# Performance work log

Measured on AMD Instinct MI355X. Metric: run time of the kernel, lower is better.

The kernel has to match this reference:

```python
import jax, jax.numpy as jnp
import numpy as np

EPS = 1e-5
K = 16
DILATION = 1

def _bn(x, g, b, axes):
    # BatchNorm in training mode: batch statistics over all axes except channel (last)
    m = jnp.mean(x, axis=axes, keepdims=True)
    v = jnp.var(x, axis=axes, keepdims=True)
    return (x - m) * jax.lax.rsqrt(v + EPS) * g + b

def _knn_idx(p, q, k):
    # p: [B,N,3], q: [B,M,3] -> indices [B,M,k] of nearest points in p for each q
    d = (jnp.sum(q * q, -1)[:, :, None]
         - 2.0 * jnp.einsum('bmc,bnc->bmn', q, p)
         + jnp.sum(p * p, -1)[:, None, :])  # [B,M,N]
    _, idx = jax.lax.top_k(-d, k)
    return jax.lax.stop_gradient(idx)

def setup_inputs() -> dict:
    key = jax.random.key(0)
    ks = jax.random.split(key, 16)
    B, N, M, Cin, Cout = 8, 8192, 2048, 64, 128
    mid, K2 = Cout // 4, K * K
    s = 0.02
    d = {
        'p': jax.random.normal(ks[0], (B, N, 3), jnp.float32),
        'q': jax.random.normal(ks[1], (B, M, 3), jnp.float32),
        'x': jax.random.normal(ks[2], (B, Cin, N), jnp.float32),
        # mlp: two 1x1 convs (3->mid->mid) each with BN
        'W1': jax.random.normal(ks[3], (mid, 3), jnp.float32) * s,
        'b1': jnp.zeros((mid,), jnp.float32),
        'g1': jnp.ones((mid,), jnp.float32), 'be1': jnp.zeros((mid,), jnp.float32),
        'W2': jax.random.normal(ks[4], (mid, mid), jnp.float32) * s,
        'b2': jnp.zeros((mid,), jnp.float32),
        'g2': jnp.ones((mid,), jnp.float32), 'be2': jnp.zeros((mid,), jnp.float32),
        # stn: conv [1,K] (3->K^2), then two 1x1 convs (K^2->K^2)
        'Ws1': jax.random.normal(ks[5], (K2, 3, K), jnp.float32) * s,
        'bs1': jnp.zeros((K2,), jnp.float32),
        'gs1': jnp.ones((K2,), jnp.float32), 'bes1': jnp.zeros((K2,), jnp.float32),
        'Ws2': jax.random.normal(ks[6], (K2, K2), jnp.float32) * s,
        'bs2': jnp.zeros((K2,), jnp.float32),
        'gs2': jnp.ones((K2,), jnp.float32), 'bes2': jnp.zeros((K2,), jnp.float32),
        'Ws3': jax.random.normal(ks[7], (K2, K2), jnp.float32) * s,
        'bs3': jnp.zeros((K2,), jnp.float32),
        # final conv [1,K]: (Cin+mid -> Cout) with BN
        'Wc': jax.random.normal(ks[8], (Cout, Cin + mid, K), jnp.float32) * s,
        'bc': jnp.zeros((Cout,), jnp.float32),
        'gc': jnp.ones((Cout,), jnp.float32), 'bec': jnp.zeros((Cout,), jnp.float32),
    }
    return d

def reference(p, q, x, W1, b1, g1, be1, W2, b2, g2, be2,
              Ws1, bs1, gs1, bes1, Ws2, bs2, gs2, bes2, Ws3, bs3,
              Wc, bc, gc, bec):
    B, M = q.shape[0], q.shape[1]
    idx = _knn_idx(p, q, K * DILATION)[..., ::DILATION]  # [B,M,K]
    # gather neighbor coords and center: p_hat [B,M,K,3]
    p_n = jax.vmap(lambda a, i: a[i])(p, idx)
    p_hat = p_n - q[:, :, None, :]
    # mlp (pointwise convs, channel-last)
    h = jax.nn.relu(_bn(jnp.einsum('bmkc,oc->bmko', p_hat, W1) + b1, g1, be1, (0, 1, 2)))
    h = jax.nn.relu(_bn(jnp.einsum('bmkc,oc->bmko', h, W2) + b2, g2, be2, (0, 1, 2)))
    # gather features: x [B,Cin,N] -> [B,M,K,Cin]
    xt = jnp.transpose(x, (0, 2, 1))
    x_n = jax.vmap(lambda a, i: a[i])(xt, idx)
    x_hat = jnp.concatenate([h, x_n], axis=-1)  # [B,M,K,mid+Cin]
    # stn -> transform T [B,M,K,K]
    t = jax.nn.relu(_bn(jnp.einsum('bmkc,ock->bmo', p_hat, Ws1) + bs1, gs1, bes1, (0, 1)))
    t = jax.nn.relu(_bn(jnp.einsum('bmi,oi->bmo', t, Ws2) + bs2, gs2, bes2, (0, 1)))
    t = jnp.einsum('bmi,oi->bmo', t, Ws3) + bs3  # [B,M,K*K]
    T = t.reshape(B, M, K, K)
    x2 = jnp.einsum('bmij,bmjc->bmic', T, x_hat)  # [B,M,K,mid+Cin]
    out = jax.nn.relu(_bn(jnp.einsum('bmkc,ock->bmo', x2, Wc) + bc, gc, bec, (0, 1)))  # [B,M,Cout]
    return (q, jnp.transpose(out, (0, 2, 1)))  # q, x:[B,Cout,M]
```

## Files before the change

kernel.cpp:

```cpp
#include <hip/hip_runtime.h>
#include <hip/hip_bf16.h>


#define EPS 1e-5f

constexpr int Bb   = 8;
constexpr int Np   = 8192;
constexpr int Mq   = 2048;
constexpr int COUT = 128;
constexpr int BM   = Bb * Mq;
constexpr int BMK  = BM * 16;
constexpr int GC   = 16;
constexpr int NC   = GC * GC * GC;
constexpr int CAP  = 320;

typedef __attribute__((ext_vector_type(8))) short short8;
typedef __attribute__((ext_vector_type(4))) float f32x4;

__device__ __forceinline__ unsigned short f2bf(float x) {
  unsigned u = __float_as_uint(x);
  u += 0x7fffu + ((u >> 16) & 1u);
  return (unsigned short)(u >> 16);
}
__device__ __forceinline__ float bf2f_lo(unsigned v) { return __uint_as_float(v << 16); }
__device__ __forceinline__ float bf2f_hi(unsigned v) { return __uint_as_float(v & 0xffff0000u); }

__device__ __forceinline__ int cell_of(float c) {
  int v = (int)floorf(c * 2.0f + 8.0f);
  return v < 0 ? 0 : (v > 15 ? 15 : v);
}

__device__ __forceinline__ unsigned enc_dist(float d) {
  unsigned uu = __float_as_uint(d);
  return uu ^ (((unsigned)(((int)uu) >> 31)) | 0x80000000u);
}

__device__ __forceinline__ void bsort64(unsigned long long& v, int lane) {
#pragma unroll
  for (int k = 2; k <= 64; k <<= 1) {
#pragma unroll
    for (int jj = k >> 1; jj > 0; jj >>= 1) {
      unsigned long long o = __shfl_xor(v, jj);
      bool keepMin = (((lane & k) == 0) == ((lane & jj) == 0));
      unsigned long long mn = v < o ? v : o;
      unsigned long long mx = v < o ? o : v;
      v = keepMin ? mn : mx;
    }
  }
}
__device__ __forceinline__ void bmerge64(unsigned long long& v, int lane) {
#pragma unroll
  for (int jj = 32; jj > 0; jj >>= 1) {
    unsigned long long o = __shfl_xor(v, jj);
    bool keepMin = ((lane & jj) == 0);
    unsigned long long mn = v < o ? v : o;
    unsigned long long mx = v < o ? o : v;
    v = keepMin ? mn : mx;
  }
}
__device__ __forceinline__ unsigned long long sort_smallest64(const unsigned long long* buf,
                                                              int C, int lane) {
  unsigned long long run = (lane < C) ? buf[lane] : ~0ULL;
  bsort64(run, lane);
  for (int b2 = 64; b2 < C; b2 += 64) {
    unsigned long long v = (b2 + lane < C) ? buf[b2 + lane] : ~0ULL;
    bsort64(v, lane);
    unsigned long long vr = __shfl_xor(v, 63);
    unsigned long long m = run < vr ? run : vr;
    bmerge64(m, lane);
    run = m;
  }
  return run;
}


__device__ __forceinline__ void bn1_compute(int o, const float* __restrict__ st,
                                            const float* __restrict__ W1,
                                            const float* __restrict__ b1,
                                            const float* __restrict__ g1,
                                            const float* __restrict__ be1,
                                            float* sc_out, float* shf_out) {
  float n = (float)BMK;
  float w0 = W1[3 * o], w1 = W1[3 * o + 1], w2 = W1[3 * o + 2], b = b1[o];
  float s0 = st[0], s1 = st[1], s2 = st[2];
  float m00 = st[3], m11 = st[4], m22 = st[5], m01 = st[6], m02 = st[7], m12 = st[8];
  float ws = (w0 * s0 + w1 * s1 + w2 * s2) / n;
  float mean = b + ws;
  float quad = w0 * w0 * m00 + w1 * w1 * m11 + w2 * w2 * m22 +
               2.f * (w0 * w1 * m01 + w0 * w2 * m02 + w1 * w2 * m12);
  float ex2 = quad / n + 2.f * b * ws + b * b;
  float var = ex2 - mean * mean;
  float sc = g1[o] * rsqrtf(var + EPS);
  *sc_out = sc;
  *shf_out = be1[o] - mean * sc + b * sc;
}

__global__ __launch_bounds__(256) void prep_kernel(const float* __restrict__ p,
                                                   const float* __restrict__ x,
                                                   const float* __restrict__ Wc,
                                                   const float* __restrict__ Ws1,
                                                   float4* __restrict__ pp4,
                                                   float* __restrict__ xt,
                                                   unsigned short* __restrict__ wcrp,
                                                   unsigned short* __restrict__ ws1r,
                                                   int* __restrict__ hist) {
  __shared__ float tile[64][65];
  int blk = blockIdx.x;
  int tid = threadIdx.x;
  if (blk < 256) {
    int i = blk * 256 + tid;
    float px = p[3 * i], py = p[3 * i + 1], pz = p[3 * i + 2];
    float pp = __fadd_rn(__fadd_rn(__fmul_rn(px, px), __fmul_rn(py, py)), __fmul_rn(pz, pz));
    pp4[i] = make_float4(px, py, pz, pp);
    int b = i >> 13;
    int cid = (cell_of(px) << 8) | (cell_of(py) << 4) | cell_of(pz);
    atomicAdd(&hist[b * NC + cid], 1);
  } else if (blk < 1280) {
    int bx = blk - 256;
    int b = bx >> 7;
    int n0 = (bx & 127) << 6;
    int nl = tid & 63;
    int r0 = tid >> 6;
    const float* xb = x + (size_t)b * 64 * Np;
    for (int c = r0; c < 64; c += 4) tile[c][nl] = xb[(size_t)c * Np + n0 + nl];
    __syncthreads();
    float* xtb = xt + (size_t)b * Np * 64;
    for (int n = r0; n < 64; n += 4) xtb[(size_t)(n0 + n) * 64 + nl] = tile[nl][n];
  } else if (blk < 2048) {
    int g = (blk - 1280) * 256 + tid;
    if (g < 128 * 1536) {
      int o = g / 1536, r = g % 1536;
      int c = r % 96, j = r / 96;
      wcrp[g] = f2bf(Wc[(size_t)o * 1536 + c * 16 + j]);
    }
  } else {
    int g = (blk - 2048) * 256 + tid;
    int o = g >> 6, i = g & 63;
    float val = 0.f;
    if (i < 48) {
      int k = i / 3, c = i - 3 * k;
      val = Ws1[(size_t)o * 48 + c * 16 + k];
    }
    unsigned short h = f2bf(val);
    float hf = __uint_as_float(((unsigned)h) << 16);
    unsigned short l = f2bf(val - hf);
    ws1r[g] = h;
    ws1r[16384 + g] = l;
  }
}

__global__ __launch_bounds__(256) void prefix_kernel(const int* __restrict__ hist,
                                                     int* __restrict__ cellstart,
                                                     int* __restrict__ cursor) {
  __shared__ int ls[256];
  int b = blockIdx.x, t = threadIdx.x;
  const int* h = hist + b * NC;
  int loc[16], s = 0;
#pragma unroll
  for (int k = 0; k < 16; ++k) { loc[k] = h[t * 16 + k]; s += loc[k]; }
  ls[t] = s;
  __syncthreads();
  for (int off = 1; off < 256; off <<= 1) {
    int v = (t >= off) ? ls[t - off] : 0;
    __syncthreads();
    ls[t] += v;
    __syncthreads();
  }
  int run = ls[t] - s;
  int* cs = cellstart + b * (NC + 1);
  int* cu = cursor + b * NC;
#pragma unroll
  for (int k = 0; k < 16; ++k) {
    cs[t * 16 + k] = run;
    cu[t * 16 + k] = run;
    run += loc[k];
  }
  if (t == 255) cs[NC] = run;
}

__global__ __launch_bounds__(256) void scatter_kernel(const float4* __restrict__ pp4,
                                                      int* __restrict__ cursor,
                                                      float4* __restrict__ sp4,
                                                      int* __restrict__ sidx) {
  int i = blockIdx.x * 256 + threadIdx.x;
  int b = i >> 13;
  float4 pv = pp4[i];
  int cid = (cell_of(pv.x) << 8) | (cell_of(pv.y) << 4) | cell_of(pv.z);
  int pos = atomicAdd(&cursor[b * NC + cid], 1);
  sp4[(size_t)b * Np + pos] = pv;
  sidx[(size_t)b * Np + pos] = i & 8191;
}

__global__ __launch_bounds__(256) void knn_kernel(const float4* __restrict__ pp4,
                                                  const float4* __restrict__ sp4,
                                                  const int* __restrict__ sidx,
                                                  const int* __restrict__ cellstart,
                                                  const float* __restrict__ q,
                                                  int* __restrict__ idx_out) {
  __shared__ unsigned long long cand[8][CAP];
  int tid = threadIdx.x;
  int wslot = tid >> 6;
  int wave = blockIdx.x * 4 + wslot;
  int lane = tid & 63;
  int q0 = wave * 2;
  int b = q0 >> 11;
  const float4* pb = pp4 + (size_t)b * Np;
  const float4* sp = sp4 + (size_t)b * Np;
  const int* sx = sidx + (size_t)b * Np;
  const int* cs = cellstart + b * (NC + 1);
  float qx[2], qy[2], qz[2], qqv[2];
#pragma unroll
  for (int j = 0; j < 2; ++j) {
    const float* qp = q + (size_t)(q0 + j) * 3;
    qx[j] = qp[0]; qy[j] = qp[1]; qz[j] = qp[2];
    qqv[j] = __fadd_rn(__fadd_rn(__fmul_rn(qx[j], qx[j]), __fmul_rn(qy[j], qy[j])),
                       __fmul_rn(qz[j], qz[j]));
  }
  float tau_f[2] = {INFINITY, INFINITY};

  for (int j = 0; j < 2; ++j) {
    int cx = cell_of(qx[j]), cy = cell_of(qy[j]), cz = cell_of(qz[j]);
    int alo = 0, blo = 0, nbw = 1, ncols = 1, zlo = 0, zhi = 0;
    int myS = 0, myE = 0;
    for (int r = 0;; ++r) {
      alo = cx - r; if (alo < 0) alo = 0;
      int ahi = cx + r; if (ahi > 15) ahi = 15;
      blo = cy - r; if (blo < 0) blo = 0;
      int bhi = cy + r; if (bhi > 15) bhi = 15;
      zlo = cz - r; if (zlo < 0) zlo = 0;
      zhi = cz + r; if (zhi > 15) zhi = 15;
      nbw = bhi - blo + 1;
      ncols = (ahi - alo + 1) * nbw;
      int total = 0;
      for (int l0 = 0; l0 < ncols; l0 += 64) {
        int l = l0 + lane;
        int sL = 0, eL = 0;
        if (l < ncols) {
          int da = l / nbw, db = l - da * nbw;
          int cbase = ((alo + da) << 8) | ((blo + db) << 4);
          sL = cs[cbase + zlo];
          eL = cs[cbase + zhi + 1];
        }
        if (l0 == 0) { myS = sL; myE = eL; }
        total += eL - sL;
      }
#pragma unroll
      for (int o = 32; o > 0; o >>= 1) total += __shfl_xor(total, o);
      if (total >= 16 || r >= 15) break;
    }
    unsigned u0 = 0xFFFFFFFFu, u1 = 0xFFFFFFFFu;
    int wcnt = 0;
    int ccen = (cx - alo) * nbw + (cy - blo);
    for (int c2 = 0; c2 < ncols && wcnt < 128; ++c2) {
      int cc = (c2 == 0) ? ccen : (c2 <= ccen ? c2 - 1 : c2);
      int s0, e;
      if (cc < 64) {
        s0 = __shfl(myS, cc);
        e = __shfl(myE, cc);
      } else {
        int da = cc / nbw, db = cc - da * nbw;
        int cbase = ((alo + da) << 8) | ((blo + db) << 4);
        s0 = cs[cbase + zlo];
        e = cs[cbase + zhi + 1];
      }
      for (int off = s0; off < e && wcnt < 128; off += 64) {
        int rem = e - off; if (rem > 64) rem = 64;
        int rot = wcnt & 63;
        int rel = (lane - rot) & 63;
        int g = wcnt + rel;
        if (rel < rem && g < 128) {
          float4 pv = sp[off + rel];
          float ee = __fmaf_rn(qz[j], pv.z, __fmaf_rn(qy[j], pv.y, __fmul_rn(qx[j], pv.x)));
          float d = __fadd_rn(__fsub_rn(qqv[j], __fmul_rn(2.0f, ee)), pv.w);
          unsigned uu = enc_dist(d);
          if (g < 64) u0 = uu; else u1 = uu;
        }
        wcnt += rem;
      }
    }
    unsigned lo = 0u, hi = 0xFF800000u;
    for (int it = 0; it < 20; ++it) {
      unsigned mid = lo + ((hi - lo) >> 1);
      int c = (int)__popcll(__ballot(u0 <= mid)) + (int)__popcll(__ballot(u1 <= mid));
      if (c >= 16) hi = mid; else lo = mid + 1;
    }
    tau_f[j] = (hi >= 0x80000000u) ? __uint_as_float(hi ^ 0x80000000u)
                                   : __uint_as_float(~hi);
  }

  int cnt[2] = {0, 0};
  unsigned long long lanebelow = (1ULL << lane) - 1ULL;
  for (int j = 0; j < 2; ++j) {
    float R = sqrtf(fmaxf(tau_f[j], 0.f) + 3e-5f) * 1.0005f;
    int ax0 = cell_of(qx[j] - R), ax1 = cell_of(qx[j] + R);
    int ay0 = cell_of(qy[j] - R), ay1 = cell_of(qy[j] + R);
    int az0 = cell_of(qz[j] - R), az1 = cell_of(qz[j] + R);
    int nby = ay1 - ay0 + 1;
    int ncols = (ax1 - ax0 + 1) * nby;
    int myS = 0, myE = 0;
    if (lane < ncols) {
      int da = lane / nby, db = lane - da * nby;
      int cbase = ((ax0 + da) << 8) | ((ay0 + db) << 4);
      myS = cs[cbase + az0];
      myE = cs[cbase + az1 + 1];
    }
    for (int cc = 0; cc < ncols; ++cc) {
      int s0, e;
      if (cc < 64) {
        s0 = __shfl(myS, cc);
        e = __shfl(myE, cc);
      } else {
        int da = cc / nby, db = cc - da * nby;
        int cbase = ((ax0 + da) << 8) | ((ay0 + db) << 4);
        s0 = cs[cbase + az0];
        e = cs[cbase + az1 + 1];
      }
      for (int off = s0; off < e; off += 64) {
        int pos = off + lane;
        bool valid = pos < e;
        float4 pv = sp[valid ? pos : s0];
        float ee = __fmaf_rn(qz[j], pv.z, __fmaf_rn(qy[j], pv.y, __fmul_rn(qx[j], pv.x)));
        float d = __fadd_rn(__fsub_rn(qqv[j], __fmul_rn(2.0f, ee)), pv.w);
        if (!valid) d = __uint_as_float(0x7FC00000u);
        unsigned long long mask = __ballot(d <= tau_f[j]);
        if (mask) {
          if (d <= tau_f[j]) {
            int oi = sx[pos];
            unsigned uu = enc_dist(d);
            int wp = cnt[j] + (int)__popcll(mask & lanebelow);
            if (wp < CAP)
              cand[wslot * 2 + j][wp] = (((unsigned long long)uu) << 32) | (unsigned)oi;
          }
          cnt[j] += (int)__popcll(mask);
        }
      }
    }
  }
  __syncthreads();

  for (int j = 0; j < 2; ++j) {
    int slot = wslot * 2 + j;
    if (cnt[j] <= CAP) {
      unsigned long long run = sort_smallest64(&cand[slot][0], cnt[j], lane);
      if (lane < 16)
        idx_out[(size_t)(q0 + j) * 16 + lane] = (int)(run & 0xffffffffULL);
    } else {
      unsigned long long kk = ~0ULL;
      float tl = tau_f[j];
      for (int base = 0; base < Np; base += 64) {
        float4 pv = pb[base + lane];
        float ee = __fmaf_rn(qz[j], pv.z, __fmaf_rn(qy[j], pv.y, __fmul_rn(qx[j], pv.x)));
        float dv = __fadd_rn(__fsub_rn(qqv[j], __fmul_rn(2.0f, ee)), pv.w);
        unsigned long long mask = __ballot(dv <= tl);
        if (mask) {
          unsigned uu = enc_dist(dv);
          unsigned long long cd = (((unsigned long long)uu) << 32) | (unsigned)(base + lane);
          do {
            int src = __ffsll((unsigned long long)mask) - 1;
            mask &= mask - 1;
            unsigned long long ck = __shfl(cd, src);
            unsigned long long up = __shfl_up(kk, 1);
            if (lane == 0) up = 0ULL;
            if (lane < 16 && ck < kk) kk = (up > ck) ? up : ck;
          } while (mask);
          unsigned long long tt = __shfl(kk, 15);
          unsigned tm = (unsigned)(tt >> 32);
          unsigned inv2 = tm ^ ((tm & 0x80000000u) ? 0x80000000u : 0xFFFFFFFFu);
          float tc = (tm == 0xFFFFFFFFu) ? INFINITY : __uint_as_float(inv2);
          if (tc < tl) tl = tc;
        }
      }
      if (lane < 16)
        idx_out[(size_t)(q0 + j) * 16 + lane] = (int)(kk & 0xffffffffULL);
    }
  }
}

__global__ __launch_bounds__(256) void phat_stats_kernel(const float4* __restrict__ pp4,
                                                         const float* __restrict__ q,
                                                         const int* __restrict__ idx,
                                                         float* __restrict__ phat,
                                                         float* __restrict__ stats) {
  float a[9];
#pragma unroll
  for (int k = 0; k < 9; ++k) a[k] = 0.f;
  int tid = threadIdx.x;
  for (int it = 0; it < 4; ++it) {
    int bmk = blockIdx.x * 256 + tid + it * 65536;
    int bm = bmk >> 4;
    int b = bm >> 11;
    int j = idx[bmk];
    float4 pv = pp4[(size_t)b * Np + j];
    const float* qp = q + (size_t)bm * 3;
    float h0 = pv.x - qp[0], h1 = pv.y - qp[1], h2 = pv.z - qp[2];
    phat[(size_t)bmk * 3 + 0] = h0;
    phat[(size_t)bmk * 3 + 1] = h1;
    phat[(size_t)bmk * 3 + 2] = h2;
    a[0] += h0; a[1] += h1; a[2] += h2;
    a[3] += h0 * h0; a[4] += h1 * h1; a[5] += h2 * h2;
    a[6] += h0 * h1; a[7] += h0 * h2; a[8] += h1 * h2;
  }
#pragma unroll
  for (int off = 32; off > 0; off >>= 1)
#pragma unroll
    for (int k = 0; k < 9; ++k) a[k] += __shfl_down(a[k], off);
  __shared__ float ls[9];
  if (tid < 9) ls[tid] = 0.f;
  __syncthreads();
  if ((tid & 63) == 0)
    for (int k = 0; k < 9; ++k) atomicAdd(&ls[k], a[k]);
  __syncthreads();
  if (tid < 9) atomicAdd(&stats[tid], ls[tid]);
}

__global__ __launch_bounds__(256) void stats2_kernel(const float* __restrict__ phat,
                                                     const float* __restrict__ stats,
                                                     const float* __restrict__ W1,
                                                     const float* __restrict__ b1,
                                                     const float* __restrict__ g1,
                                                     const float* __restrict__ be1,
                                                     const float* __restrict__ W2,
                                                     const float* __restrict__ b2,
                                                     float* __restrict__ stats2) {
  __shared__ float hsh[256 * 36];
  __shared__ float w2s[32 * 33];
  __shared__ float w1s[96], sc1[32], sh1[32], b2s[32], ls[64];
  int tid = threadIdx.x;
  if (tid < 32) {
    bn1_compute(tid, stats, W1, b1, g1, be1, &sc1[tid], &sh1[tid]);
    b2s[tid] = b2[tid];
  }
  if (tid < 96) w1s[tid] = W1[tid];
  if (tid < 64) ls[tid] = 0.f;
  for (int e = tid; e < 1024; e += 256) w2s[(e >> 5) * 33 + (e & 31)] = W2[e];
  __syncthreads();
  {
    int bmk = blockIdx.x * 256 + tid;
    float h0 = phat[(size_t)bmk * 3], hy = phat[(size_t)bmk * 3 + 1], hz = phat[(size_t)bmk * 3 + 2];
#pragma unroll
    for (int o4 = 0; o4 < 8; ++o4) {
      float4 r;
      float* rp = (float*)&r;
#pragma unroll
      for (int u = 0; u < 4; ++u) {
        int o = o4 * 4 + u;
        float t = w1s[3 * o] * h0 + w1s[3 * o + 1] * hy + w1s[3 * o + 2] * hz;
        rp[u] = fmaxf(0.f, t * sc1[o] + sh1[o]);
      }
      *(float4*)&hsh[tid * 36 + o4 * 4] = r;
    }
  }
  __syncthreads();
  int oc = tid & 31, grp = tid >> 5;
  float wrow[32];
#pragma unroll
  for (int c = 0; c < 32; ++c) wrow[c] = w2s[oc * 33 + c];
  float bias = b2s[oc];
  float ss = 0.f, qq = 0.f;
  for (int r = 0; r < 32; ++r) {
    int row = grp * 32 + r;
    float a = bias;
    const float4* hr = (const float4*)&hsh[row * 36];
#pragma unroll
    for (int c4 = 0; c4 < 8; ++c4) {
      float4 hv = hr[c4];
      a += hv.x * wrow[c4 * 4 + 0];
      a += hv.y * wrow[c4 * 4 + 1];
      a += hv.z * wrow[c4 * 4 + 2];
      a += hv.w * wrow[c4 * 4 + 3];
    }
    ss += a;
    qq += a * a;
  }
  atomicAdd(&ls[oc], ss);
  atomicAdd(&ls[32 + oc], qq);
  __syncthreads();
  if (tid < 64) atomicAdd(&stats2[tid], ls[tid]);
}

__global__ __launch_bounds__(256) void stn1_kernel(const float* __restrict__ phat,
                                                   const unsigned short* __restrict__ ws1r,
                                                   const float* __restrict__ bs1,
                                                   float* __restrict__ pt1,
                                                   float* __restrict__ spt1) {
  __shared__ unsigned short Ah[64 * 72], Al[64 * 72], Bh[128 * 72], Bl[128 * 72];
  __shared__ float ls[256];
  int tid = threadIdx.x;
  ls[tid] = 0.f;
  int mb = blockIdx.x >> 1, nb = blockIdx.x & 1;
  int bm0 = mb * 64, o0 = nb * 128;
  {
    int zr = tid >> 2, zc = 48 + (tid & 3) * 4;
    *(unsigned long long*)&Ah[zr * 72 + zc] = 0ULL;
    *(unsigned long long*)&Al[zr * 72 + zc] = 0ULL;
  }
  {
    int ar = tid >> 2, aseg = tid & 3;
    const float* Ap = phat + (size_t)(bm0 + ar) * 48 + aseg * 12;
    float4 v0 = *(const float4*)(Ap);
    float4 v1 = *(const float4*)(Ap + 4);
    float4 v2 = *(const float4*)(Ap + 8);
    float av[12] = {v0.x, v0.y, v0.z, v0.w, v1.x, v1.y, v1.z, v1.w, v2.x, v2.y, v2.z, v2.w};
    unsigned long long ph[3] = {0ULL, 0ULL, 0ULL}, pl[3] = {0ULL, 0ULL, 0ULL};
#pragma unroll
    for (int t = 0; t < 12; ++t) {
      unsigned short h = f2bf(av[t]);
      float hf = __uint_as_float(((unsigned)h) << 16);
      unsigned short l = f2bf(av[t] - hf);
      ph[t >> 2] |= ((unsigned long long)h) << ((t & 3) * 16);
      pl[t >> 2] |= ((unsigned long long)l) << ((t & 3) * 16);
    }
    int base = ar * 72 + aseg * 12;
#pragma unroll
    for (int t4 = 0; t4 < 3; ++t4) {
      *(unsigned long long*)&Ah[base + t4 * 4] = ph[t4];
      *(unsigned long long*)&Al[base + t4 * 4] = pl[t4];
    }
  }
#pragma unroll
  for (int pass = 0; pass < 4; ++pass) {
    int g = pass * 2048 + tid * 8;
    int br = g >> 6, i2 = g & 63;
    short8 vh = *(const short8*)&ws1r[(size_t)(o0 + br) * 64 + i2];
    short8 vl = *(const short8*)&ws1r[16384 + (size_t)(o0 + br) * 64 + i2];
    *(short8*)&Bh[br * 72 + i2] = vh;
    *(short8*)&Bl[br * 72 + i2] = vl;
  }
  __syncthreads();
  int wid = tid >> 6, lane = tid & 63;
  int wm = wid >> 1, wn = wid & 1;
  int mh = lane & 15, quad = lane >> 4;
  f32x4 acc[2][4];
#pragma unroll
  for (int a = 0; a < 2; ++a)
#pragma unroll
    for (int bq = 0; bq < 4; ++bq) acc[a][bq] = (f32x4){0.f, 0.f, 0.f, 0.f};
#pragma unroll
  for (int kc = 0; kc < 2; ++kc) {
    int ko = kc * 32 + quad * 8;
#pragma unroll
    for (int mt = 0; mt < 2; ++mt) {
      short8 ah = *(const short8*)&Ah[(wm * 32 + mt * 16 + mh) * 72 + ko];
      short8 al = *(const short8*)&Al[(wm * 32 + mt * 16 + mh) * 72 + ko];
#pragma unroll
      for (int nt = 0; nt < 4; ++nt) {
        short8 bh = *(const short8*)&Bh[(wn * 64 + nt * 16 + mh) * 72 + ko];
        short8 bl = *(const short8*)&Bl[(wn * 64 + nt * 16 + mh) * 72 + ko];
        acc[mt][nt] = __builtin_amdgcn_mfma_f32_16x16x32_bf16(ah, bh, acc[mt][nt], 0, 0, 0);
        acc[mt][nt] = __builtin_amdgcn_mfma_f32_16x16x32_bf16(ah, bl, acc[mt][nt], 0, 0, 0);
        acc[mt][nt] = __builtin_amdgcn_mfma_f32_16x16x32_bf16(al, bh, acc[mt][nt], 0, 0, 0);
      }
    }
  }
#pragma unroll
  for (int mt = 0; mt < 2; ++mt)
#pragma unroll
    for (int nt = 0; nt < 4; ++nt) {
      int colL = wn * 64 + nt * 16 + mh;
      int col = o0 + colL;
      float bvv = bs1[col];
      float ps = 0.f, pq = 0.f;
#pragma unroll
      for (int r = 0; r < 4; ++r) {
        float val = acc[mt][nt][r] + bvv;
        pt1[(size_t)(bm0 + wm * 32 + mt * 16 + quad * 4 + r) * 256 + col] = val;
        ps += val;
        pq += val * val;
      }
      atomicAdd(&ls[colL], ps);
      atomicAdd(&ls[128 + colL], pq);
    }
  __syncthreads();
  if (tid < 128) {
    atomicAdd(&spt1[o0 + tid], ls[tid]);
    atomicAdd(&spt1[256 + o0 + tid], ls[128 + tid]);
  }
}

__global__ __launch_bounds__(256) void stn_mm_kernel(const float* __restrict__ in,
                                                     const float* __restrict__ sums,
                                                     const float* __restrict__ gg,
                                                     const float* __restrict__ be,
                                                     const float* __restrict__ W,
                                                     const float* __restrict__ bias,
                                                     float* __restrict__ out,
                                                     float* __restrict__ outstats,
                                                     int do_stats) {
  __shared__ unsigned short As[64 * 40], Bs[128 * 40];
  __shared__ float scA[256], shA[256], ls[256];
  int tid = threadIdx.x;
  ls[tid] = 0.f;
  {
    float n = (float)BM;
    float mean = sums[tid] / n;
    float var = sums[256 + tid] / n - mean * mean;
    float s = gg[tid] * rsqrtf(var + EPS);
    scA[tid] = s;
    shA[tid] = be[tid] - mean * s;
  }
  int mb = blockIdx.x >> 1, nb = blockIdx.x & 1;
  int bm0 = mb * 64, o0 = nb * 128;
  int wid = tid >> 6, lane = tid & 63;
  int wm = wid >> 1, wn = wid & 1;
  int mh = lane & 15, quad = lane >> 4;
  f32x4 acc[2][4];
#pragma unroll
  for (int a = 0; a < 2; ++a)
#pragma unroll
    for (int bq = 0; bq < 4; ++bq) acc[a][bq] = (f32x4){0.f, 0.f, 0.f, 0.f};
  int ar = tid >> 2, aseg = tid & 3;
  const float* Ag = in + (size_t)(bm0 + ar) * 256 + aseg * 8;
  int aoff = ar * 40 + aseg * 8;
  int ci = aseg * 8;
  for (int i0 = 0; i0 < 256; i0 += 32) {
    __syncthreads();
    float4 v0 = *(const float4*)(Ag + i0);
    float4 v1 = *(const float4*)(Ag + i0 + 4);
    float av[8] = {v0.x, v0.y, v0.z, v0.w, v1.x, v1.y, v1.z, v1.w};
    short8 ap;
#pragma unroll
    for (int k = 0; k < 8; ++k)
      ap[k] = (short)f2bf(fmaxf(0.f, av[k] * scA[i0 + ci + k] + shA[i0 + ci + k]));
    *(short8*)&As[aoff] = ap;
#pragma unroll
    for (int jb = 0; jb < 2; ++jb) {
      int br = jb * 64 + ar;
      const float* Bg = W + (size_t)(o0 + br) * 256 + aseg * 8;
      float4 u0 = *(const float4*)(Bg + i0);
      float4 u1 = *(const float4*)(Bg + i0 + 4);
      float bv[8] = {u0.x, u0.y, u0.z, u0.w, u1.x, u1.y, u1.z, u1.w};
      short8 bp;
#pragma unroll
      for (int k = 0; k < 8; ++k) bp[k] = (short)f2bf(bv[k]);
      *(short8*)&Bs[br * 40 + aseg * 8] = bp;
    }
    __syncthreads();
#pragma unroll
    for (int mt = 0; mt < 2; ++mt) {
      short8 af = *(const short8*)&As[(wm * 32 + mt * 16 + mh) * 40 + quad * 8];
#pragma unroll
      for (int nt = 0; nt < 4; ++nt) {
        short8 bf = *(const short8*)&Bs[(wn * 64 + nt * 16 + mh) * 40 + quad * 8];
        acc[mt][nt] = __builtin_amdgcn_mfma_f32_16x16x32_bf16(af, bf, acc[mt][nt], 0, 0, 0);
      }
    }
  }
#pragma unroll
  for (int mt = 0; mt < 2; ++mt)
#pragma unroll
    for (int nt = 0; nt < 4; ++nt) {
      int colL = wn * 64 + nt * 16 + mh;
      int col = o0 + colL;
      float bvv = bias[col];
      float ps = 0.f, pq = 0.f;
#pragma unroll
      for (int r = 0; r < 4; ++r) {
        float val = acc[mt][nt][r] + bvv;
        out[(size_t)(bm0 + wm * 32 + mt * 16 + quad * 4 + r) * 256 + col] = val;
        ps += val;
        pq += val * val;
      }
      if (do_stats) {
        atomicAdd(&ls[colL], ps);
        atomicAdd(&ls[128 + colL], pq);
      }
    }
  if (do_stats) {
    __syncthreads();
    if (tid < 128) {
      atomicAdd(&outstats[o0 + tid], ls[tid]);
      atomicAdd(&outstats[256 + o0 + tid], ls[128 + tid]);
    }
  }
}

__global__ __launch_bounds__(256) void xhat_x2_kernel(const float* __restrict__ phat,
                                                      const float* __restrict__ stats,
                                                      const float* __restrict__ stats2,
                                                      const float* __restrict__ W1,
                                                      const float* __restrict__ b1,
                                                      const float* __restrict__ g1,
                                                      const float* __restrict__ be1,
                                                      const float* __restrict__ W2,
                                                      const float* __restrict__ b2,
                                                      const float* __restrict__ g2,
                                                      const float* __restrict__ be2,
                                                      const float* __restrict__ xt,
                                                      const int* __restrict__ idx,
                                                      const float* __restrict__ Tbuf,
                                                      unsigned short* __restrict__ x2) {
  __shared__ unsigned xh[256 * 17];
  __shared__ float w1s[96], w2s[32 * 33], sc1[32], sh1[32], sc2[32], sh2[32];
  int tid = threadIdx.x;
  if (tid < 32) {
    bn1_compute(tid, stats, W1, b1, g1, be1, &sc1[tid], &sh1[tid]);
    float n = (float)BMK;
    float mean = stats2[tid] / n;
    float var = stats2[32 + tid] / n - mean * mean;
    float s = g2[tid] * rsqrtf(var + EPS);
    sc2[tid] = s;
    sh2[tid] = be2[tid] - mean * s + b2[tid] * s;
  }
  if (tid < 96) w1s[tid] = W1[tid];
  for (int e = tid; e < 1024; e += 256) w2s[(e >> 5) * 33 + (e & 31)] = W2[e];
  __syncthreads();
  int bm0 = blockIdx.x * 16;
  int b = bm0 >> 11;
  int bml = tid >> 4, j = tid & 15;
  int bmk = (bm0 + bml) * 16 + j;
  unsigned h2p[16];
  {
    float h0 = phat[(size_t)bmk * 3], hy = phat[(size_t)bmk * 3 + 1], hz = phat[(size_t)bmk * 3 + 2];
    float h1v[32];
#pragma unroll
    for (int o = 0; o < 32; ++o) {
      float t = w1s[3 * o] * h0 + w1s[3 * o + 1] * hy + w1s[3 * o + 2] * hz;
      h1v[o] = fmaxf(0.f, t * sc1[o] + sh1[o]);
    }
#pragma unroll
    for (int o4 = 0; o4 < 8; ++o4) {
      float r[4];
#pragma unroll
      for (int u = 0; u < 4; ++u) {
        int o = o4 * 4 + u;
        float a = 0.f;
#pragma unroll
        for (int c = 0; c < 32; ++c) a += h1v[c] * w2s[o * 33 + c];
        r[u] = fmaxf(0.f, a * sc2[o] + sh2[o]);
      }
      h2p[o4 * 2] = (unsigned)f2bf(r[0]) | (((unsigned)f2bf(r[1])) << 16);
      h2p[o4 * 2 + 1] = (unsigned)f2bf(r[2]) | (((unsigned)f2bf(r[3])) << 16);
    }
  }
  int jx = idx[bmk];
  const float4* xr = (const float4*)(xt + ((size_t)b * Np + jx) * 64);
  float Tr[16];
  {
    const float4* tg = (const float4*)(Tbuf + (size_t)(bm0 + bml) * 256 + j * 16);
#pragma unroll
    for (int w4 = 0; w4 < 4; ++w4) {
      float4 tv = tg[w4];
      Tr[w4 * 4 + 0] = tv.x; Tr[w4 * 4 + 1] = tv.y;
      Tr[w4 * 4 + 2] = tv.z; Tr[w4 * 4 + 3] = tv.w;
    }
  }
  unsigned* dst32 = (unsigned*)(x2 + (size_t)bmk * 96);
#pragma unroll
  for (int ch = 0; ch < 3; ++ch) {
    if (ch == 0) {
#pragma unroll
      for (int t = 0; t < 16; ++t) xh[tid * 17 + t] = h2p[t];
    } else {
      float4 xv[8];
#pragma unroll
      for (int t = 0; t < 8; ++t) xv[t] = xr[(ch - 1) * 8 + t];
#pragma unroll
      for (int t = 0; t < 8; ++t) {
        xh[tid * 17 + t * 2] = (unsigned)f2bf(xv[t].x) | (((unsigned)f2bf(xv[t].y)) << 16);
        xh[tid * 17 + t * 2 + 1] = (unsigned)f2bf(xv[t].z) | (((unsigned)f2bf(xv[t].w)) << 16);
      }
    }
    __syncthreads();
    float acc[32];
#pragma unroll
    for (int cc = 0; cc < 32; ++cc) acc[cc] = 0.f;
#pragma unroll
    for (int jj = 0; jj < 16; ++jj) {
      const unsigned* xr2 = &xh[(bml * 16 + jj) * 17];
      float t = Tr[jj];
#pragma unroll
      for (int cc = 0; cc < 16; ++cc) {
        unsigned uv = xr2[cc];
        acc[cc * 2] += t * bf2f_lo(uv);
        acc[cc * 2 + 1] += t * bf2f_hi(uv);
      }
    }
#pragma unroll
    for (int cc = 0; cc < 16; ++cc)
      dst32[ch * 16 + cc] = (unsigned)f2bf(acc[cc * 2]) | (((unsigned)f2bf(acc[cc * 2 + 1])) << 16);
    __syncthreads();
  }
}

__global__ __launch_bounds__(256) void preout_kernel(const unsigned short* __restrict__ x2,
                                                     const unsigned short* __restrict__ Wcrp,
                                                     const float* __restrict__ bc,
                                                     float* __restrict__ pout,
                                                     float* __restrict__ spout) {
  __shared__ unsigned short As[64 * 40], Bs[128 * 40];
  __shared__ float ls[256];
  int tid = threadIdx.x;
  ls[tid] = 0.f;
  int bm0 = blockIdx.x * 64;
  int wid = tid >> 6, lane = tid & 63;
  int wm = wid >> 1, wn = wid & 1;
  int mh = lane & 15, quad = lane >> 4;
  f32x4 acc[2][4];
#pragma unroll
  for (int a = 0; a < 2; ++a)
#pragma unroll
    for (int bq = 0; bq < 4; ++bq) acc[a][bq] = (f32x4){0.f, 0.f, 0.f, 0.f};
  int ar = tid >> 2, aseg = tid & 3;
  const unsigned short* Ag = x2 + (size_t)(bm0 + ar) * 1536 + aseg * 8;
  const unsigned short* Bg0 = Wcrp + (size_t)ar * 1536 + aseg * 8;
  const unsigned short* Bg1 = Wcrp + (size_t)(64 + ar) * 1536 + aseg * 8;
  int aoff = ar * 40 + aseg * 8;
  short8 a_pre = *(const short8*)Ag;
  short8 b_pre0 = *(const short8*)Bg0;
  short8 b_pre1 = *(const short8*)Bg1;
  for (int i0 = 0; i0 < 1536; i0 += 32) {
    __syncthreads();
    *(short8*)&As[aoff] = a_pre;
    *(short8*)&Bs[aoff] = b_pre0;
    *(short8*)&Bs[64 * 40 + aoff] = b_pre1;
    __syncthreads();
    if (i0 + 32 < 1536) {
      a_pre = *(const short8*)(Ag + i0 + 32);
      b_pre0 = *(const short8*)(Bg0 + i0 + 32);
      b_pre1 = *(const short8*)(Bg1 + i0 + 32);
    }
#pragma unroll
    for (int mt = 0; mt < 2; ++mt) {
      short8 af = *(const short8*)&As[(wm * 32 + mt * 16 + mh) * 40 + quad * 8];
#pragma unroll
      for (int nt = 0; nt < 4; ++nt) {
        short8 bf = *(const short8*)&Bs[(wn * 64 + nt * 16 + mh) * 40 + quad * 8];
        acc[mt][nt] = __builtin_amdgcn_mfma_f32_16x16x32_bf16(af, bf, acc[mt][nt], 0, 0, 0);
      }
    }
  }
#pragma unroll
  for (int mt = 0; mt < 2; ++mt)
#pragma unroll
    for (int nt = 0; nt < 4; ++nt) {
      int col = wn * 64 + nt * 16 + mh;
      float bvv = bc[col];
      float ps = 0.f, pq = 0.f;
#pragma unroll
      for (int r = 0; r < 4; ++r) {
        float val = acc[mt][nt][r] + bvv;
        pout[(size_t)(bm0 + wm * 32 + mt * 16 + quad * 4 + r) * 128 + col] = val;
        ps += val;
        pq += val * val;
      }
      atomicAdd(&ls[col], ps);
      atomicAdd(&ls[128 + col], pq);
    }
  __syncthreads();
  atomicAdd(&spout[tid], ls[tid]);
}

__global__ __launch_bounds__(256) void final_kernel(const float* __restrict__ q,
                                                    const float* __restrict__ pout,
                                                    const float* __restrict__ scs,
                                                    const float* __restrict__ gc,
                                                    const float* __restrict__ bec,
                                                    float* __restrict__ dout) {
  __shared__ float ldsT[128 * 65];
  int blk = blockIdx.x;
  int tid = threadIdx.x;
  if (blk < 192) {
    int g = blk * 256 + tid;
    dout[g] = q[g];
    return;
  }
  int blk2 = blk - 192;
  int b = blk2 >> 5;
  int m0 = (blk2 & 31) * 64;
  int row = tid >> 2, seg = tid & 3;
  const float4* src = (const float4*)(pout + ((size_t)(b * Mq) + m0 + row) * 128 + seg * 32);
#pragma unroll
  for (int k4 = 0; k4 < 8; ++k4) {
    float4 v = src[k4];
    int o = seg * 32 + k4 * 4;
    ldsT[(o + 0) * 65 + row] = v.x;
    ldsT[(o + 1) * 65 + row] = v.y;
    ldsT[(o + 2) * 65 + row] = v.z;
    ldsT[(o + 3) * 65 + row] = v.w;
  }
  __syncthreads();
  int lane = tid & 63, wv = tid >> 6;
  float n = (float)BM;
  float* base = dout + (size_t)BM * 3 + (size_t)b * COUT * Mq + m0;
#pragma unroll
  for (int rep = 0; rep < 32; ++rep) {
    int o = wv * 32 + rep;
    float mean = scs[o] / n;
    float var = scs[128 + o] / n - mean * mean;
    float s = gc[o] * rsqrtf(var + EPS);
    float shv = bec[o] - mean * s;
    float v = ldsT[o * 65 + lane];
    base[(size_t)o * Mq + lane] = fmaxf(0.f, v * s + shv);
  }
}

extern "C" void kernel_launch(void* const* d_in, const int* in_sizes, int n_in, void* d_out,
                              int out_size, void* d_ws, size_t ws_size, hipStream_t stream) {
  const float* p = (const float*)d_in[0];
  const float* q = (const float*)d_in[1];
  const float* x = (const float*)d_in[2];
  const float* W1 = (const float*)d_in[3];
  const float* b1 = (const float*)d_in[4];
  const float* g1 = (const float*)d_in[5];
  const float* be1 = (const float*)d_in[6];
  const float* W2 = (const float*)d_in[7];
  const float* b2 = (const float*)d_in[8];
  const float* g2 = (const float*)d_in[9];
  const float* be2 = (const float*)d_in[10];
  const float* Ws1 = (const float*)d_in[11];
  const float* bs1 = (const float*)d_in[12];
  const float* gs1 = (const float*)d_in[13];
  const float* bes1 = (const float*)d_in[14];
  const float* Ws2 = (const float*)d_in[15];
  const float* bs2 = (const float*)d_in[16];
  const float* gs2 = (const float*)d_in[17];
  const float* bes2 = (const float*)d_in[18];
  const float* Ws3 = (const float*)d_in[19];
  const float* bs3 = (const float*)d_in[20];
  const float* Wc = (const float*)d_in[21];
  const float* bc = (const float*)d_in[22];
  const float* gc = (const float*)d_in[23];
  const float* bec = (const float*)d_in[24];
  float* dout = (float*)d_out;

  char* ws = (char*)d_ws;
  float* stats = (float*)ws;
  size_t off = 8192;
  float4* pp4 = (float4*)(ws + off);  off += (size_t)Bb * Np * 16;
  int* idxb = (int*)(ws + off);       off += (size_t)BMK * 4;
  float* xt = (float*)(ws + off);     off += (size_t)Bb * Np * 64 * 4;
  float* phat = (float*)(ws + off);   off += (size_t)BMK * 3 * 4;
  float* pt1 = (float*)(ws + off);    off += (size_t)BM * 256 * 4;
  float* pt2 = (float*)(ws + off);    off += (size_t)BM * 256 * 4;
  float* Tb = (float*)(ws + off);     off += (size_t)BM * 256 * 4;
  float* pout = (float*)(ws + off);   off += (size_t)BM * 128 * 4;
  unsigned short* wcrp = (unsigned short*)(ws + off); off += (size_t)1536 * 128 * 2;
  unsigned short* x2 = (unsigned short*)(ws + off);   off += (size_t)BM * 1536 * 2;
  int* hist = (int*)(ws + off);       off += (size_t)Bb * NC * 4;
  int* cursor = (int*)(ws + off);     off += (size_t)Bb * NC * 4;
  int* cellstart = (int*)(ws + off);  off += (size_t)Bb * (NC + 1) * 4;
  float4* sp4 = (float4*)(ws + off);  off += (size_t)Bb * Np * 16;
  int* sidx = (int*)(ws + off);       off += (size_t)Bb * Np * 4;
  unsigned short* ws1r = (unsigned short*)(ws + off); off += (size_t)2 * 256 * 64 * 2;

  hipMemsetAsync(stats, 0, 8192, stream);
  hipMemsetAsync(hist, 0, (size_t)Bb * NC * 4, stream);
  hipLaunchKernelGGL(prep_kernel, dim3(2112), dim3(256), 0, stream, p, x, Wc, Ws1, pp4, xt, wcrp, ws1r, hist);
  hipLaunchKernelGGL(prefix_kernel, dim3(8), dim3(256), 0, stream, hist, cellstart, cursor);
  hipLaunchKernelGGL(scatter_kernel, dim3(256), dim3(256), 0, stream, pp4, cursor, sp4, sidx);
  hipLaunchKernelGGL(knn_kernel, dim3(2048), dim3(256), 0, stream, pp4, sp4, sidx, cellstart, q, idxb);
  hipLaunchKernelGGL(phat_stats_kernel, dim3(256), dim3(256), 0, stream, pp4, q, idxb, phat, stats);
  hipLaunchKernelGGL(stn1_kernel, dim3(512), dim3(256), 0, stream, phat, ws1r, bs1, pt1, stats + 128);
  hipLaunchKernelGGL(stats2_kernel, dim3(1024), dim3(256), 0, stream, phat, stats, W1, b1, g1, be1, W2, b2, stats + 16);
  hipLaunchKernelGGL(stn_mm_kernel, dim3(512), dim3(256), 0, stream, pt1, stats + 128, gs1, bes1, Ws2, bs2, pt2, stats + 640, 1);
  hipLaunchKernelGGL(stn_mm_kernel, dim3(512), dim3(256), 0, stream, pt2, stats + 640, gs2, bes2, Ws3, bs3, Tb, (float*)nullptr, 0);
  hipLaunchKernelGGL(xhat_x2_kernel, dim3(1024), dim3(256), 0, stream, phat, stats, stats + 16,
                     W1, b1, g1, be1, W2, b2, g2, be2, xt, idxb, Tb, x2);
  hipLaunchKernelGGL(preout_kernel, dim3(256), dim3(256), 0, stream, x2, wcrp, bc, pout, stats + 1152);
  hipLaunchKernelGGL(final_kernel, dim3(448), dim3(256), 0, stream, q, pout, stats + 1152, gc, bec, dout);
}
```

Baseline: 379.9 us.

## Restructure T·x_hat product so each thread owns a channel column, not a row

Each thread now computes one channel pair (or quad) for all 16 output neighbours of its query, instead of one output row across all channels. T rows are staged in shared memory, and neighbour features are gathered straight from global memory as contiguous float4s with bf16 rounding. Only one sync is needed now, the three-chunk xh staging loop is gone, and the W1/W2 shared-memory copies are replaced by direct global reads. The cost is less coalesced global loads and stores (each thread writes strided 4-byte words across 16 rows) and more shared reads of T.

```diff
diff --git a/kernel.cpp b/kernel.cpp
--- a/kernel.cpp
+++ b/kernel.cpp
@@ -24,6 +24,9 @@
 }
 __device__ __forceinline__ float bf2f_lo(unsigned v) { return __uint_as_float(v << 16); }
 __device__ __forceinline__ float bf2f_hi(unsigned v) { return __uint_as_float(v & 0xffff0000u); }
+__device__ __forceinline__ float bfround(float x) {
+  return __uint_as_float(((unsigned)f2bf(x)) << 16);
+}
 
 __device__ __forceinline__ int cell_of(float c) {
   int v = (int)floorf(c * 2.0f + 8.0f);
@@ -690,7 +693,8 @@
                                                       const float* __restrict__ Tbuf,
                                                       unsigned short* __restrict__ x2) {
   __shared__ unsigned xh[256 * 17];
-  __shared__ float w1s[96], w2s[32 * 33], sc1[32], sh1[32], sc2[32], sh2[32];
+  __shared__ float Tst[256 * 16];
+  __shared__ float sc1[32], sh1[32], sc2[32], sh2[32];
   int tid = threadIdx.x;
   if (tid < 32) {
     bn1_compute(tid, stats, W1, b1, g1, be1, &sc1[tid], &sh1[tid]);
@@ -701,20 +705,17 @@
     sc2[tid] = s;
     sh2[tid] = be2[tid] - mean * s + b2[tid] * s;
   }
-  if (tid < 96) w1s[tid] = W1[tid];
-  for (int e = tid; e < 1024; e += 256) w2s[(e >> 5) * 33 + (e & 31)] = W2[e];
   __syncthreads();
   int bm0 = blockIdx.x * 16;
   int b = bm0 >> 11;
   int bml = tid >> 4, j = tid & 15;
   int bmk = (bm0 + bml) * 16 + j;
-  unsigned h2p[16];
   {
     float h0 = phat[(size_t)bmk * 3], hy = phat[(size_t)bmk * 3 + 1], hz = phat[(size_t)bmk * 3 + 2];
     float h1v[32];
 #pragma unroll
     for (int o = 0; o < 32; ++o) {
-      float t = w1s[3 * o] * h0 + w1s[3 * o + 1] * hy + w1s[3 * o + 2] * hz;
+      float t = W1[3 * o] * h0 + W1[3 * o + 1] * hy + W1[3 * o + 2] * hz;
       h1v[o] = fmaxf(0.f, t * sc1[o] + sh1[o]);
     }
 #pragma unroll
@@ -725,60 +726,71 @@
         int o = o4 * 4 + u;
         float a = 0.f;
 #pragma unroll
-        for (int c = 0; c < 32; ++c) a += h1v[c] * w2s[o * 33 + c];
+        for (int c = 0; c < 32; ++c) a += h1v[c] * W2[o * 32 + c];
         r[u] = fmaxf(0.f, a * sc2[o] + sh2[o]);
       }
-      h2p[o4 * 2] = (unsigned)f2bf(r[0]) | (((unsigned)f2bf(r[1])) << 16);
-      h2p[o4 * 2 + 1] = (unsigned)f2bf(r[2]) | (((unsigned)f2bf(r[3])) << 16);
-    }
-  }
-  int jx = idx[bmk];
-  const float4* xr = (const float4*)(xt + ((size_t)b * Np + jx) * 64);
-  float Tr[16];
+      xh[tid * 17 + o4 * 2] = (unsigned)f2bf(r[0]) | (((unsigned)f2bf(r[1])) << 16);
+      xh[tid * 17 + o4 * 2 + 1] = (unsigned)f2bf(r[2]) | (((unsigned)f2bf(r[3])) << 16);
+    }
+    const float4* tg = (const float4*)(Tbuf + (size_t)(bm0 + bml) * 256 + j * 16);
+    float4* td = (float4*)&Tst[tid * 16];
+    td[0] = tg[0]; td[1] = tg[1]; td[2] = tg[2]; td[3] = tg[3];
+  }
+  __syncthreads();
+  int cl = j;
   {
-    const float4* tg = (const float4*)(Tbuf + (size_t)(bm0 + bml) * 256 + j * 16);
-#pragma unroll
-    for (int w4 = 0; w4 < 4; ++w4) {
-      float4 tv = tg[w4];
-      Tr[w4 * 4 + 0] = tv.x; Tr[w4 * 4 + 1] = tv.y;
-      Tr[w4 * 4 + 2] = tv.z; Tr[w4 * 4 + 3] = tv.w;
-    }
-  }
-  unsigned* dst32 = (unsigned*)(x2 + (size_t)bmk * 96);
-#pragma unroll
-  for (int ch = 0; ch < 3; ++ch) {
-    if (ch == 0) {
-#pragma unroll
-      for (int t = 0; t < 16; ++t) xh[tid * 17 + t] = h2p[t];
-    } else {
-      float4 xv[8];
-#pragma unroll
-      for (int t = 0; t < 8; ++t) xv[t] = xr[(ch - 1) * 8 + t];
-#pragma unroll
-      for (int t = 0; t < 8; ++t) {
-        xh[tid * 17 + t * 2] = (unsigned)f2bf(xv[t].x) | (((unsigned)f2bf(xv[t].y)) << 16);
-        xh[tid * 17 + t * 2 + 1] = (unsigned)f2bf(xv[t].z) | (((unsigned)f2bf(xv[t].w)) << 16);
-      }
-    }
-    __syncthreads();
-    float acc[32];
-#pragma unroll
-    for (int cc = 0; cc < 32; ++cc) acc[cc] = 0.f;
+    float vlo[16], vhi[16];
 #pragma unroll
     for (int jj = 0; jj < 16; ++jj) {
-      const unsigned* xr2 = &xh[(bml * 16 + jj) * 17];
-      float t = Tr[jj];
-#pragma unroll
-      for (int cc = 0; cc < 16; ++cc) {
-        unsigned uv = xr2[cc];
-        acc[cc * 2] += t * bf2f_lo(uv);
-        acc[cc * 2 + 1] += t * bf2f_hi(uv);
-      }
-    }
-#pragma unroll
-    for (int cc = 0; cc < 16; ++cc)
-      dst32[ch * 16 + cc] = (unsigned)f2bf(acc[cc * 2]) | (((unsigned)f2bf(acc[cc * 2 + 1])) << 16);
-    __syncthreads();
+      unsigned uv = xh[(bml * 16 + jj) * 17 + cl];
+      vlo[jj] = bf2f_lo(uv);
+      vhi[jj] = bf2f_hi(uv);
+    }
+    for (int jo = 0; jo < 16; ++jo) {
+      const float4* tr4 = (const float4*)&Tst[(bml * 16 + jo) * 16];
+      float4 ta = tr4[0], tb = tr4[1], tc = tr4[2], tdd = tr4[3];
+      float trow[16] = {ta.x, ta.y, ta.z, ta.w, tb.x, tb.y, tb.z, tb.w,
+                        tc.x, tc.y, tc.z, tc.w, tdd.x, tdd.y, tdd.z, tdd.w};
+      float a0 = 0.f, a1 = 0.f;
+#pragma unroll
+      for (int jj = 0; jj < 16; ++jj) {
+        a0 += trow[jj] * vlo[jj];
+        a1 += trow[jj] * vhi[jj];
+      }
+      unsigned* dst = (unsigned*)(x2 + (size_t)((bm0 + bml) * 16 + jo) * 96);
+      dst[cl] = (unsigned)f2bf(a0) | (((unsigned)f2bf(a1)) << 16);
+    }
+  }
+  {
+    const int* idxrow = idx + (size_t)(bm0 + bml) * 16;
+    float v0[16], v1[16], v2[16], v3[16];
+#pragma unroll
+    for (int jj = 0; jj < 16; ++jj) {
+      int jx = idxrow[jj];
+      float4 xv = *(const float4*)(xt + ((size_t)b * Np + jx) * 64 + cl * 4);
+      v0[jj] = bfround(xv.x);
+      v1[jj] = bfround(xv.y);
+      v2[jj] = bfround(xv.z);
+      v3[jj] = bfround(xv.w);
+    }
+    for (int jo = 0; jo < 16; ++jo) {
+      const float4* tr4 = (const float4*)&Tst[(bml * 16 + jo) * 16];
+      float4 ta = tr4[0], tb = tr4[1], tc = tr4[2], tdd = tr4[3];
+      float trow[16] = {ta.x, ta.y, ta.z, ta.w, tb.x, tb.y, tb.z, tb.w,
+                        tc.x, tc.y, tc.z, tc.w, tdd.x, tdd.y, tdd.z, tdd.w};
+      float a0 = 0.f, a1 = 0.f, a2 = 0.f, a3 = 0.f;
+#pragma unroll
+      for (int jj = 0; jj < 16; ++jj) {
+        float t = trow[jj];
+        a0 += t * v0[jj];
+        a1 += t * v1[jj];
+        a2 += t * v2[jj];
+        a3 += t * v3[jj];
+      }
+      unsigned* dst = (unsigned*)(x2 + (size_t)((bm0 + bml) * 16 + jo) * 96);
+      dst[16 + cl * 2] = (unsigned)f2bf(a0) | (((unsigned)f2bf(a1)) << 16);
+      dst[17 + cl * 2] = (unsigned)f2bf(a2) | (((unsigned)f2bf(a3)) << 16);
+    }
   }
 }
 
```

Measured after the change: 357.0 us. -6.0%, faster.
